# Kernel optimization log

Measured on AMD Instinct MI355X. Metric: run time of the kernel, lower is better.

The kernel has to match this reference:

```python
import jax, jax.numpy as jnp
import numpy as np

NUM_EXPERTS = 64
TOP_K = 2


def setup_inputs() -> dict:
    key = jax.random.key(0)
    k1, k2 = jax.random.split(key)
    hidden_states = jax.random.normal(k1, (4, 8192, 2048), dtype=jnp.float32)
    # torch nn.Linear weight layout: (num_experts, hidden)
    W = jax.random.normal(k2, (NUM_EXPERTS, 2048), dtype=jnp.float32) * 0.02
    return {"hidden_states": hidden_states, "W": W}


def reference(hidden_states, W):
    b, s, h = hidden_states.shape
    x = hidden_states.reshape(-1, h)                      # (T, H), T = b*s
    logits = jnp.einsum('th,eh->te', x, W)                # (T, E) skinny gate GEMM
    # eval mode: no gaussian noise added
    top_vals, indices = jax.lax.top_k(logits, TOP_K)      # (T, K)
    gates = jax.nn.softmax(top_vals, axis=-1)
    gates = gates.reshape(b, s, TOP_K)
    indices = indices.reshape(b, s, TOP_K)
    # load-balance auxiliary loss (faithful to source, incl. probs>0 mask)
    probs = jax.nn.softmax(logits, axis=-1)               # (T, E)
    mean_probs = probs.mean(axis=0)                       # (E,)
    routing_probs = (probs > 0).astype(logits.dtype).mean(axis=0)  # (E,)
    load_balance_loss = NUM_EXPERTS * jnp.sum(mean_probs * routing_probs)
    return (gates, indices, load_balance_loss)
```

## Files before the change

### kernel.cpp

```cpp
#include <hip/hip_runtime.h>
#include <math.h>

#define H      2048
#define E      64
#define MTOK   16
#define BTOK   64
#define KC     64
#define KC4    16
#define NCHUNK (H / KC)
#define T_TOK  32768
#define GATES_OFF   0
#define IDX_OFF     65536
#define LOSS_OFF    131072

__global__ void transpose_w_kernel(const float* __restrict__ W, float* __restrict__ Wt,
                                   float* __restrict__ accum) {
    int id = blockIdx.x * 256 + threadIdx.x;
    if (blockIdx.x == 0 && threadIdx.x < 128) accum[threadIdx.x] = 0.f;
    int e = id >> 11;
    int h = id & 2047;
    Wt[(h >> 2) * 256 + (e << 2) + (h & 3)] = W[id];
}

__device__ __forceinline__ void async_copy16(const float* g, void* l) {
    __builtin_amdgcn_global_load_lds(
        (const __attribute__((address_space(1))) unsigned int*)g,
        (__attribute__((address_space(3))) unsigned int*)l,
        16, 0, 0);
}

__global__ __launch_bounds__(256) void gate_main_kernel(
        const float* __restrict__ x,
        const float4* __restrict__ wt4,
        float* __restrict__ out,
        float* __restrict__ accum)
{
    __shared__ float4 xtile[2][BTOK * KC4];
    __shared__ float  redP[4][64];
    __shared__ float  redC[4][64];

    const int tid  = threadIdx.x;
    const int lane = tid & 63;
    const int wave = tid >> 6;
    const int tokBase = blockIdx.x * BTOK;

    const float* xg = x + (size_t)tokBase * H;

    auto stage = [&](int c, int b) {
#pragma unroll
        for (int j = 0; j < 4; ++j) {
            int f = tid + j * 256;
            int token = f >> 4;
            int k4 = f & 15;
            async_copy16(xg + (size_t)token * H + c * KC + k4 * 4, &xtile[b][f]);
        }
    };

    float acc[MTOK];
#pragma unroll
    for (int m = 0; m < MTOK; ++m) acc[m] = 0.f;

    stage(0, 0);

    for (int c = 0; c < NCHUNK; ++c) {
        const int b = c & 1;
        __syncthreads();
        if (c + 1 < NCHUNK) stage(c + 1, b ^ 1);

        const float4* xw = &xtile[b][wave * (MTOK * KC4)];
        const float4* wp = wt4 + (size_t)c * (KC4 * E) + lane;
#pragma unroll
        for (int k4 = 0; k4 < KC4; ++k4) {
            float4 wv = wp[k4 * E];
#pragma unroll
            for (int m = 0; m < MTOK; ++m) {
                float4 xv = xw[m * KC4 + k4];
                float a = acc[m];
                a = fmaf(xv.x, wv.x, a);
                a = fmaf(xv.y, wv.y, a);
                a = fmaf(xv.z, wv.z, a);
                a = fmaf(xv.w, wv.w, a);
                acc[m] = a;
            }
        }
    }

    float sumP = 0.f, cntP = 0.f;
    const int tokW = tokBase + wave * MTOK;

#pragma unroll
    for (int m = 0; m < MTOK; ++m) {
        float v = acc[m];

        float vmax = v;
#pragma unroll
        for (int d = 32; d > 0; d >>= 1) vmax = fmaxf(vmax, __shfl_xor(vmax, d, 64));
        float ex = expf(v - vmax);
        float s = ex;
#pragma unroll
        for (int d = 32; d > 0; d >>= 1) s += __shfl_xor(s, d, 64);
        float p = ex / s;
        sumP += p;
        cntP += (p > 0.f) ? 1.f : 0.f;

        float v1 = v; int i1 = lane;
#pragma unroll
        for (int d = 32; d > 0; d >>= 1) {
            float ov = __shfl_xor(v1, d, 64);
            int   oi = __shfl_xor(i1, d, 64);
            if (ov > v1 || (ov == v1 && oi < i1)) { v1 = ov; i1 = oi; }
        }
        float v2 = (lane == i1) ? -INFINITY : v; int i2 = lane;
#pragma unroll
        for (int d = 32; d > 0; d >>= 1) {
            float ov = __shfl_xor(v2, d, 64);
            int   oi = __shfl_xor(i2, d, 64);
            if (ov > v2 || (ov == v2 && oi < i2)) { v2 = ov; i2 = oi; }
        }

        if (lane == 0) {
            int token = tokW + m;
            float t  = expf(v2 - v1);
            float d  = 1.f / (1.f + t);
            out[GATES_OFF + 2 * token]     = d;
            out[GATES_OFF + 2 * token + 1] = t * d;
            out[IDX_OFF   + 2 * token]     = (float)i1;
            out[IDX_OFF   + 2 * token + 1] = (float)i2;
        }
    }

    redP[wave][lane] = sumP;
    redC[wave][lane] = cntP;
    __syncthreads();
    if (wave == 0) {
        float sp = redP[0][lane] + redP[1][lane] + redP[2][lane] + redP[3][lane];
        float sc = redC[0][lane] + redC[1][lane] + redC[2][lane] + redC[3][lane];
        atomicAdd(&accum[lane], sp);
        atomicAdd(&accum[E + lane], sc);
    }
}

__global__ void gate_final_kernel(const float* __restrict__ accum, float* __restrict__ out) {
    int lane = threadIdx.x;
    const float invT = 1.f / (float)T_TOK;
    float mean_p   = accum[lane] * invT;
    float routing  = accum[E + lane] * invT;
    float term = mean_p * routing;
#pragma unroll
    for (int d = 32; d > 0; d >>= 1) term += __shfl_xor(term, d, 64);
    if (lane == 0) out[LOSS_OFF] = 64.f * term;
}

extern "C" void kernel_launch(void* const* d_in, const int* in_sizes, int n_in,
                              void* d_out, int out_size, void* d_ws, size_t ws_size,
                              hipStream_t stream) {
    const float* x = (const float*)d_in[0];
    const float* W = (const float*)d_in[1];
    float* out   = (float*)d_out;
    float* accum = (float*)d_ws;
    float* Wt    = (float*)d_ws + 128;

    transpose_w_kernel<<<512, 256, 0, stream>>>(W, Wt, accum);
    gate_main_kernel<<<T_TOK / BTOK, 256, 0, stream>>>(x, (const float4*)Wt, out, accum);
    gate_final_kernel<<<1, 64, 0, stream>>>(accum, out);
}
```

Baseline: 585.8 us.

## Rewrite gate GEMM as token-per-lane with split-K across waves

Replaces the LDS-staged, expert-per-lane gate GEMM with a layout where each lane owns one token and accumulates all 64 expert logits in registers. The hidden dimension is split across 8 waves, with a swizzled LDS tree reduction to combine partial sums. W is read directly via wave-uniform addresses, which removes the transpose kernel and the cross-lane shuffle softmax/top-k in favour of per-thread serial loops. The cost is heavy register pressure (64 accumulators plus prefetched x vectors) and uncoalesced per-token row reads of x. It also uses the fast __expf.

```diff
diff --git a/kernel.cpp b/kernel.cpp
--- a/kernel.cpp
+++ b/kernel.cpp
@@ -1,150 +1,166 @@
 #include <hip/hip_runtime.h>
 #include <math.h>
 
-#define H      2048
-#define E      64
-#define MTOK   16
-#define BTOK   64
-#define KC     64
-#define KC4    16
-#define NCHUNK (H / KC)
-#define T_TOK  32768
+#define H       2048
+#define E       64
+#define NCHUNK  16
+#define T_TOK   32768
 #define GATES_OFF   0
 #define IDX_OFF     65536
 #define LOSS_OFF    131072
 
-__global__ void transpose_w_kernel(const float* __restrict__ W, float* __restrict__ Wt,
-                                   float* __restrict__ accum) {
-    int id = blockIdx.x * 256 + threadIdx.x;
-    if (blockIdx.x == 0 && threadIdx.x < 128) accum[threadIdx.x] = 0.f;
-    int e = id >> 11;
-    int h = id & 2047;
-    Wt[(h >> 2) * 256 + (e << 2) + (h & 3)] = W[id];
+__global__ void zero_accum_kernel(float* __restrict__ accum) {
+    accum[threadIdx.x] = 0.f;
 }
 
-__device__ __forceinline__ void async_copy16(const float* g, void* l) {
-    __builtin_amdgcn_global_load_lds(
-        (const __attribute__((address_space(1))) unsigned int*)g,
-        (__attribute__((address_space(3))) unsigned int*)l,
-        16, 0, 0);
-}
-
-__global__ __launch_bounds__(256) void gate_main_kernel(
+__global__ __launch_bounds__(512) void gate_main_kernel(
         const float* __restrict__ x,
-        const float4* __restrict__ wt4,
+        const float* __restrict__ W,
         float* __restrict__ out,
         float* __restrict__ accum)
 {
-    __shared__ float4 xtile[2][BTOK * KC4];
-    __shared__ float  redP[4][64];
-    __shared__ float  redC[4][64];
+    __shared__ float redf[4][64][64];
 
-    const int tid  = threadIdx.x;
-    const int lane = tid & 63;
-    const int wave = tid >> 6;
-    const int tokBase = blockIdx.x * BTOK;
+    const int tid   = threadIdx.x;
+    const int lane  = tid & 63;
+    const int wv    = tid >> 6;
+    const int wvu   = __builtin_amdgcn_readfirstlane(wv);
+    const int token = blockIdx.x * 64 + lane;
 
-    const float* xg = x + (size_t)tokBase * H;
+    const float4* xrow = (const float4*)(x + (size_t)token * H) + wvu * 4;
+    const float4* Wv   = (const float4*)W;
 
-    auto stage = [&](int c, int b) {
+    float acc[E];
 #pragma unroll
-        for (int j = 0; j < 4; ++j) {
-            int f = tid + j * 256;
-            int token = f >> 4;
-            int k4 = f & 15;
-            async_copy16(xg + (size_t)token * H + c * KC + k4 * 4, &xtile[b][f]);
+    for (int e = 0; e < E; ++e) acc[e] = 0.f;
+
+    float4 xc0 = xrow[0], xc1 = xrow[1], xc2 = xrow[2], xc3 = xrow[3];
+
+    for (int c = 0; c < NCHUNK; ++c) {
+        const int cn = (c + 1 < NCHUNK) ? (c + 1) * 32 : c * 32;
+        float4 xn0 = xrow[cn + 0];
+        float4 xn1 = xrow[cn + 1];
+        float4 xn2 = xrow[cn + 2];
+        float4 xn3 = xrow[cn + 3];
+
+        const float4* wp = Wv + c * 32 + wvu * 4;
+#pragma unroll
+        for (int e = 0; e < E; ++e) {
+            float4 w0 = wp[e * 512 + 0];
+            float4 w1 = wp[e * 512 + 1];
+            float4 w2 = wp[e * 512 + 2];
+            float4 w3 = wp[e * 512 + 3];
+            float a = acc[e];
+            a = fmaf(xc0.x, w0.x, a);
+            a = fmaf(xc0.y, w0.y, a);
+            a = fmaf(xc0.z, w0.z, a);
+            a = fmaf(xc0.w, w0.w, a);
+            a = fmaf(xc1.x, w1.x, a);
+            a = fmaf(xc1.y, w1.y, a);
+            a = fmaf(xc1.z, w1.z, a);
+            a = fmaf(xc1.w, w1.w, a);
+            a = fmaf(xc2.x, w2.x, a);
+            a = fmaf(xc2.y, w2.y, a);
+            a = fmaf(xc2.z, w2.z, a);
+            a = fmaf(xc2.w, w2.w, a);
+            a = fmaf(xc3.x, w3.x, a);
+            a = fmaf(xc3.y, w3.y, a);
+            a = fmaf(xc3.z, w3.z, a);
+            a = fmaf(xc3.w, w3.w, a);
+            acc[e] = a;
+        }
+        xc0 = xn0; xc1 = xn1; xc2 = xn2; xc3 = xn3;
+    }
+
+    auto dump = [&](int b) {
+#pragma unroll
+        for (int e4 = 0; e4 < 16; ++e4) {
+            int col = (e4 ^ (lane & 15)) * 4;
+            *(float4*)&redf[b][lane][col] =
+                make_float4(acc[e4*4], acc[e4*4+1], acc[e4*4+2], acc[e4*4+3]);
+        }
+    };
+    auto gather = [&](int b) {
+#pragma unroll
+        for (int e4 = 0; e4 < 16; ++e4) {
+            int col = (e4 ^ (lane & 15)) * 4;
+            float4 v = *(const float4*)&redf[b][lane][col];
+            acc[e4*4]   += v.x;
+            acc[e4*4+1] += v.y;
+            acc[e4*4+2] += v.z;
+            acc[e4*4+3] += v.w;
         }
     };
 
-    float acc[MTOK];
+    if (wv >= 4) dump(wv - 4);
+    __syncthreads();
+    if (wv < 4) gather(wv);
+    __syncthreads();
+    if (wv == 2 || wv == 3) dump(wv - 2);
+    __syncthreads();
+    if (wv < 2) gather(wv);
+    __syncthreads();
+    if (wv == 1) dump(0);
+    __syncthreads();
+
+    if (wv == 0) {
+        gather(0);
+
+        float v1 = acc[0]; int i1 = 0;
+        float v2 = -INFINITY; int i2 = 0;
 #pragma unroll
-    for (int m = 0; m < MTOK; ++m) acc[m] = 0.f;
+        for (int e = 1; e < E; ++e) {
+            float v = acc[e];
+            if (v > v1)      { v2 = v1; i2 = i1; v1 = v; i1 = e; }
+            else if (v > v2) { v2 = v;  i2 = e; }
+        }
 
-    stage(0, 0);
-
-    for (int c = 0; c < NCHUNK; ++c) {
-        const int b = c & 1;
-        __syncthreads();
-        if (c + 1 < NCHUNK) stage(c + 1, b ^ 1);
-
-        const float4* xw = &xtile[b][wave * (MTOK * KC4)];
-        const float4* wp = wt4 + (size_t)c * (KC4 * E) + lane;
+        float s = 0.f;
 #pragma unroll
-        for (int k4 = 0; k4 < KC4; ++k4) {
-            float4 wv = wp[k4 * E];
-#pragma unroll
-            for (int m = 0; m < MTOK; ++m) {
-                float4 xv = xw[m * KC4 + k4];
-                float a = acc[m];
-                a = fmaf(xv.x, wv.x, a);
-                a = fmaf(xv.y, wv.y, a);
-                a = fmaf(xv.z, wv.z, a);
-                a = fmaf(xv.w, wv.w, a);
-                acc[m] = a;
-            }
-        }
-    }
-
-    float sumP = 0.f, cntP = 0.f;
-    const int tokW = tokBase + wave * MTOK;
+        for (int e = 0; e < E; ++e) { acc[e] = __expf(acc[e] - v1); s += acc[e]; }
+        float inv = 1.f / s;
 
 #pragma unroll
-    for (int m = 0; m < MTOK; ++m) {
-        float v = acc[m];
-
-        float vmax = v;
-#pragma unroll
-        for (int d = 32; d > 0; d >>= 1) vmax = fmaxf(vmax, __shfl_xor(vmax, d, 64));
-        float ex = expf(v - vmax);
-        float s = ex;
-#pragma unroll
-        for (int d = 32; d > 0; d >>= 1) s += __shfl_xor(s, d, 64);
-        float p = ex / s;
-        sumP += p;
-        cntP += (p > 0.f) ? 1.f : 0.f;
-
-        float v1 = v; int i1 = lane;
-#pragma unroll
-        for (int d = 32; d > 0; d >>= 1) {
-            float ov = __shfl_xor(v1, d, 64);
-            int   oi = __shfl_xor(i1, d, 64);
-            if (ov > v1 || (ov == v1 && oi < i1)) { v1 = ov; i1 = oi; }
-        }
-        float v2 = (lane == i1) ? -INFINITY : v; int i2 = lane;
-#pragma unroll
-        for (int d = 32; d > 0; d >>= 1) {
-            float ov = __shfl_xor(v2, d, 64);
-            int   oi = __shfl_xor(i2, d, 64);
-            if (ov > v2 || (ov == v2 && oi < i2)) { v2 = ov; i2 = oi; }
+        for (int e4 = 0; e4 < 16; ++e4) {
+            int col = (e4 ^ (lane & 15)) * 4;
+            float p0 = acc[e4*4]   * inv;
+            float p1 = acc[e4*4+1] * inv;
+            float p2 = acc[e4*4+2] * inv;
+            float p3 = acc[e4*4+3] * inv;
+            *(float4*)&redf[0][lane][col] = make_float4(p0, p1, p2, p3);
+            *(float4*)&redf[1][lane][col] = make_float4(p0 > 0.f ? 1.f : 0.f,
+                                                        p1 > 0.f ? 1.f : 0.f,
+                                                        p2 > 0.f ? 1.f : 0.f,
+                                                        p3 > 0.f ? 1.f : 0.f);
         }
 
-        if (lane == 0) {
-            int token = tokW + m;
-            float t  = expf(v2 - v1);
-            float d  = 1.f / (1.f + t);
-            out[GATES_OFF + 2 * token]     = d;
-            out[GATES_OFF + 2 * token + 1] = t * d;
-            out[IDX_OFF   + 2 * token]     = (float)i1;
-            out[IDX_OFF   + 2 * token + 1] = (float)i2;
+        float t = __expf(v2 - v1);
+        float d = 1.f / (1.f + t);
+        *(float2*)&out[GATES_OFF + 2 * token] = make_float2(d, t * d);
+        *(float2*)&out[IDX_OFF   + 2 * token] = make_float2((float)i1, (float)i2);
+    }
+    __syncthreads();
+
+    {
+        const int e = lane;
+        float sp = 0.f, sc = 0.f;
+#pragma unroll
+        for (int t0 = 0; t0 < 8; ++t0) {
+            int tt  = wv * 8 + t0;
+            int idx = (((e >> 2) ^ (tt & 15)) << 2) + (e & 3);
+            sp += redf[0][tt][idx];
+            sc += redf[1][tt][idx];
         }
-    }
-
-    redP[wave][lane] = sumP;
-    redC[wave][lane] = cntP;
-    __syncthreads();
-    if (wave == 0) {
-        float sp = redP[0][lane] + redP[1][lane] + redP[2][lane] + redP[3][lane];
-        float sc = redC[0][lane] + redC[1][lane] + redC[2][lane] + redC[3][lane];
-        atomicAdd(&accum[lane], sp);
-        atomicAdd(&accum[E + lane], sc);
+        atomicAdd(&accum[e],     sp);
+        atomicAdd(&accum[E + e], sc);
     }
 }
 
 __global__ void gate_final_kernel(const float* __restrict__ accum, float* __restrict__ out) {
     int lane = threadIdx.x;
     const float invT = 1.f / (float)T_TOK;
-    float mean_p   = accum[lane] * invT;
-    float routing  = accum[E + lane] * invT;
+    float mean_p  = accum[lane] * invT;
+    float routing = accum[E + lane] * invT;
     float term = mean_p * routing;
 #pragma unroll
     for (int d = 32; d > 0; d >>= 1) term += __shfl_xor(term, d, 64);
@@ -158,9 +174,8 @@
     const float* W = (const float*)d_in[1];
     float* out   = (float*)d_out;
     float* accum = (float*)d_ws;
-    float* Wt    = (float*)d_ws + 128;
 
-    transpose_w_kernel<<<512, 256, 0, stream>>>(W, Wt, accum);
-    gate_main_kernel<<<T_TOK / BTOK, 256, 0, stream>>>(x, (const float4*)Wt, out, accum);
+    zero_accum_kernel<<<1, 128, 0, stream>>>(accum);
+    gate_main_kernel<<<T_TOK / 64, 512, 0, stream>>>(x, W, out, accum);
     gate_final_kernel<<<1, 64, 0, stream>>>(accum, out);
 }
```

Measured after the change: 1.104 ms. +88.4%, slower.
